# Kernel optimization log

Measured on AMD Instinct MI355X. Metric: run time of the kernel, lower is better.

Reference implementation:

```python
import math
import jax, jax.numpy as jnp
import numpy as np

B, T, E, H = 4, 2048, 1024, 16
D = E // H          # head_dim = 64
F = D // 2          # num_pairs = 32
FREQ_SIGMA = 1.0


def _build_spiral_frequencies(num_heads, num_pairs, freq_sigma):
    indices = np.arange(num_pairs, dtype=np.float32) + 0.5
    magnitudes = np.linspace(freq_sigma / max(num_pairs, 1), freq_sigma, num_pairs, dtype=np.float32)
    head_phases = np.linspace(0.0, 2.0 * math.pi, num_heads + 1, dtype=np.float32)[:-1][:, None]
    golden = (1.0 + math.sqrt(5.0)) / 2.0
    y = np.clip(1.0 - 2.0 * indices / float(num_pairs), -1.0, 1.0)
    radius = np.sqrt(np.clip(1.0 - y ** 2, 0.0, None))
    theta = (2.0 * math.pi * indices / golden)[None, :] + head_phases
    x = radius[None, :] * np.cos(theta)
    z = radius[None, :] * np.sin(theta)
    directions = np.stack([x, np.broadcast_to(y[None, :], (num_heads, num_pairs)), z], axis=-1)
    return (directions * magnitudes[None, :, None]).astype(np.float32)  # (H, F, 3)


def setup_inputs() -> dict:
    key = jax.random.key(0)
    ks = jax.random.split(key, 4)
    query = jax.random.normal(ks[0], (B, T, E), dtype=jnp.float32)
    positions = jax.random.normal(ks[1], (B, T, 3), dtype=jnp.float32)
    in_proj_weight = jax.random.normal(ks[2], (3 * E, E), dtype=jnp.float32) * (1.0 / math.sqrt(E))
    in_proj_bias = jnp.zeros((3 * E,), dtype=jnp.float32)
    out_proj_weight = jax.random.normal(ks[3], (E, E), dtype=jnp.float32) * (1.0 / math.sqrt(E))
    out_proj_bias = jnp.zeros((E,), dtype=jnp.float32)
    freqs = jnp.asarray(_build_spiral_frequencies(H, F, FREQ_SIGMA))
    return dict(query=query, positions=positions, in_proj_weight=in_proj_weight,
                in_proj_bias=in_proj_bias, out_proj_weight=out_proj_weight,
                out_proj_bias=out_proj_bias, freqs=freqs)


def _apply_rotary(x, positions, freqs):
    # x: (B, H, T, D), positions: (B, T, 3), freqs: (H, F, 3)
    angles = jnp.einsum('btd,hfd->bhtf', positions.astype(jnp.float32), freqs.astype(jnp.float32))
    cos = jnp.cos(angles).astype(x.dtype)
    sin = jnp.sin(angles).astype(x.dtype)
    xr = x.reshape(*x.shape[:-1], F, 2)
    x0, x1 = xr[..., 0], xr[..., 1]
    rotated = jnp.stack((x0 * cos - x1 * sin, x0 * sin + x1 * cos), axis=-1)
    return rotated.reshape(x.shape)  # rotary_dim == head_dim here


def reference(query, positions, in_proj_weight, in_proj_bias, out_proj_weight, out_proj_bias, freqs):
    b, t, e = query.shape
    h = freqs.shape[0]
    d = e // h
    # QKV projections (self-attention: all from query)
    q = query @ in_proj_weight[:e].T + in_proj_bias[:e]
    k = query @ in_proj_weight[e:2 * e].T + in_proj_bias[e:2 * e]
    v = query @ in_proj_weight[2 * e:].T + in_proj_bias[2 * e:]
    # split heads -> (B, H, T, D)
    q = q.reshape(b, t, h, d).transpose(0, 2, 1, 3)
    k = k.reshape(b, t, h, d).transpose(0, 2, 1, 3)
    v = v.reshape(b, t, h, d).transpose(0, 2, 1, 3)
    q = _apply_rotary(q, positions, freqs)
    k = _apply_rotary(k, positions, freqs)
    # SDPA
    scale = 1.0 / math.sqrt(d)
    scores = jnp.einsum('bhqd,bhkd->bhqk', q, k) * scale
    attn = jax.nn.softmax(scores, axis=-1)
    out = jnp.einsum('bhqk,bhkd->bhqd', attn, v)
    out = out.transpose(0, 2, 1, 3).reshape(b, t, e)
    return out @ out_proj_weight.T + out_proj_bias
```

## Files before the change

kernel.cpp:

```cpp
#include <hip/hip_runtime.h>
#include <math.h>

#define NB 4
#define NT 2048
#define NE 1024
#define NH 16
#define ND 64
#define NF 32

typedef _Float16 half8 __attribute__((ext_vector_type(8)));
typedef _Float16 half4 __attribute__((ext_vector_type(4)));
typedef _Float16 half2v __attribute__((ext_vector_type(2)));
typedef unsigned short ushort8v __attribute__((ext_vector_type(8)));
typedef unsigned int uint4v __attribute__((ext_vector_type(4)));
typedef float f32x4 __attribute__((ext_vector_type(4)));
typedef float f32x16 __attribute__((ext_vector_type(16)));
#define MFMA16(a, b, c) __builtin_amdgcn_mfma_f32_16x16x32_f16(a, b, c, 0, 0, 0)
#define MFMA32(a, b, c) __builtin_amdgcn_mfma_f32_32x32x16_f16(a, b, c, 0, 0, 0)

__device__ __forceinline__ float fast_exp2(float x) {
    float r;
    asm volatile("v_exp_f32 %0, %1" : "=v"(r) : "v"(x));
    return r;
}

__global__ __launch_bounds__(256)
void cvt_kernel(const float* __restrict__ X, const float* __restrict__ Wi,
                const float* __restrict__ Wo,
                _Float16* __restrict__ Xh, _Float16* __restrict__ Wih,
                _Float16* __restrict__ Woh)
{
    const size_t NX = (size_t)8388608, NWI = 3145728, NWO = 1048576;
    const size_t TOT = (NX + NWI + NWO) / 8;
    for (size_t gidx = (size_t)blockIdx.x*256 + threadIdx.x; gidx < TOT;
         gidx += (size_t)gridDim.x*256) {
        size_t i = gidx*8;
        const float* src; _Float16* dst; size_t off;
        if (i < NX)            { src = X;  dst = Xh;  off = i; }
        else if (i < NX + NWI) { src = Wi; dst = Wih; off = i - NX; }
        else                   { src = Wo; dst = Woh; off = i - NX - NWI; }
        float4 a = *(const float4*)(src + off);
        float4 b = *(const float4*)(src + off + 4);
        half8 h;
        h[0]=(_Float16)a.x; h[1]=(_Float16)a.y; h[2]=(_Float16)a.z; h[3]=(_Float16)a.w;
        h[4]=(_Float16)b.x; h[5]=(_Float16)b.y; h[6]=(_Float16)b.z; h[7]=(_Float16)b.w;
        *(half8*)(dst + off) = h;
    }
}

__global__ __launch_bounds__(256)
void qkv_mfma_kernel(const _Float16* __restrict__ Ah,
                     const _Float16* __restrict__ Bh,
                     const float* __restrict__ bias,
                     const float* __restrict__ pos,
                     const float* __restrict__ freqs,
                     _Float16* __restrict__ Qh,
                     _Float16* __restrict__ Kh,
                     _Float16* __restrict__ Vh)
{
    __shared__ _Float16 Ash[128*32];
    __shared__ _Float16 Bsh[128*32];

    const int tid = threadIdx.x;
    const int wid = tid >> 6, lane = tid & 63;
    const int ln = lane & 15, g = lane >> 4;
    const int wrow = wid >> 1, wcol = wid & 1;
    const int m0 = blockIdx.x * 128, n0 = blockIdx.y * 128;

    const int r0 = tid >> 2, s0 = tid & 3;
    const int k8 = s0 ^ ((r0 >> 1) & 3);
    const _Float16* gA0 = Ah + (size_t)(m0 + r0)      * NE + k8*8;
    const _Float16* gA1 = Ah + (size_t)(m0 + r0 + 64) * NE + k8*8;
    const _Float16* gB0 = Bh + (size_t)(n0 + r0)      * NE + k8*8;
    const _Float16* gB1 = Bh + (size_t)(n0 + r0 + 64) * NE + k8*8;

    const int xr = g ^ ((ln >> 1) & 3);

    f32x4 acc[4][4];
    #pragma unroll
    for (int i = 0; i < 4; ++i)
        #pragma unroll
        for (int j = 0; j < 4; ++j) acc[i][j] = (f32x4){0.f,0.f,0.f,0.f};

    half8 va0 = *(const half8*)gA0;
    half8 va1 = *(const half8*)gA1;
    half8 vb0 = *(const half8*)gB0;
    half8 vb1 = *(const half8*)gB1;

    for (int kt = 0; kt < NE; kt += 32) {
        if (kt) __syncthreads();
        *(half8*)&Ash[tid*8]       = va0;
        *(half8*)&Ash[(tid+256)*8] = va1;
        *(half8*)&Bsh[tid*8]       = vb0;
        *(half8*)&Bsh[(tid+256)*8] = vb1;
        __syncthreads();
        const int kn = kt + 32;
        if (kn < NE) {
            va0 = *(const half8*)(gA0 + kn);
            va1 = *(const half8*)(gA1 + kn);
            vb0 = *(const half8*)(gB0 + kn);
            vb1 = *(const half8*)(gB1 + kn);
        }
        half8 af[4], bf[4];
        #pragma unroll
        for (int mf = 0; mf < 4; ++mf)
            af[mf] = *(const half8*)&Ash[(wrow*64 + mf*16 + ln)*32 + xr*8];
        #pragma unroll
        for (int nf = 0; nf < 4; ++nf)
            bf[nf] = *(const half8*)&Bsh[(wcol*64 + nf*16 + ln)*32 + xr*8];
        __builtin_amdgcn_s_setprio(1);
        #pragma unroll
        for (int mf = 0; mf < 4; ++mf)
            #pragma unroll
            for (int nf = 0; nf < 4; ++nf)
                acc[mf][nf] = MFMA16(af[mf], bf[nf], acc[mf][nf]);
        __builtin_amdgcn_s_setprio(0);
    }

    const int sec = n0 >> 10;
    _Float16* dst = (sec == 0) ? Qh : (sec == 1) ? Kh : Vh;

    float cb[4], fx[4], fy[4], fz[4];
    int hh[4], dd[4];
    #pragma unroll
    for (int nf = 0; nf < 4; ++nf) {
        const int col = n0 + wcol*64 + nf*16 + ln;
        cb[nf] = bias[col];
        const int e = col & 1023;
        hh[nf] = e >> 6; dd[nf] = e & 63;
        if (sec != 2) {
            const float* fq = freqs + ((size_t)hh[nf]*NF + (dd[nf] >> 1))*3;
            fx[nf] = fq[0]; fy[nf] = fq[1]; fz[nf] = fq[2];
        }
    }
    const float sgn = (ln & 1) ? 1.0f : -1.0f;
    const float qs  = (sec == 0) ? 0.125f * 1.4426950408889634f : 1.0f;

    #pragma unroll
    for (int mf = 0; mf < 4; ++mf) {
        #pragma unroll
        for (int r = 0; r < 4; ++r) {
            const int m = m0 + wrow*64 + mf*16 + g*4 + r;
            const int b = m >> 11, t = m & 2047;
            if (sec == 2) {
                #pragma unroll
                for (int nf = 0; nf < 4; ++nf)
                    dst[((size_t)(b*NH + hh[nf])*NT + t)*ND + dd[nf]] =
                        (_Float16)(acc[mf][nf][r] + cb[nf]);
            } else {
                const float px = pos[(size_t)m*3 + 0];
                const float py = pos[(size_t)m*3 + 1];
                const float pz = pos[(size_t)m*3 + 2];
                #pragma unroll
                for (int nf = 0; nf < 4; ++nf) {
                    const float x  = acc[mf][nf][r] + cb[nf];
                    const float xo = __shfl_xor(x, 1);
                    const float ang = px*fx[nf] + py*fy[nf] + pz*fz[nf];
                    float sn, cs;
                    __sincosf(ang, &sn, &cs);
                    const float out = (x*cs + sgn*xo*sn) * qs;
                    dst[((size_t)(b*NH + hh[nf])*NT + t)*ND + dd[nf]] = (_Float16)out;
                }
            }
        }
    }
}

__global__ __launch_bounds__(256)
void attn_mfma_kernel(const _Float16* __restrict__ Qg, const _Float16* __restrict__ Kg,
                      const _Float16* __restrict__ Vg, _Float16* __restrict__ Og)
{
    __shared__ _Float16 Ks[64][68];
    __shared__ _Float16 VsT[64][68];

    const int tid  = threadIdx.x;
    const int wid  = tid >> 6;
    const int lane = tid & 63;
    const int m31  = lane & 31;
    const int hi   = lane >> 5;
    const int bh   = blockIdx.x;
    const int qt   = blockIdx.y;
    const int b = bh >> 4, h = bh & 15;
    const _Float16* Qp = Qg + (size_t)bh * NT * ND;
    const _Float16* Kp = Kg + (size_t)bh * NT * ND;
    const _Float16* Vp = Vg + (size_t)bh * NT * ND;

    const int qrow_g = qt*128 + wid*32 + m31;

    half8 qfr[4];
    #pragma unroll
    for (int c = 0; c < 4; ++c)
        qfr[c] = *(const half8*)(Qp + (size_t)qrow_g*ND + 16*c + 8*hi);

    f32x16 o[2];
    #pragma unroll
    for (int e = 0; e < 16; ++e) { o[0][e] = 0.f; o[1][e] = 0.f; }
    float m_i = -INFINITY, l_i = 0.0f;

    const int sr  = tid >> 2;
    const int sc0 = (tid & 3) * 16;
    const int dp  = tid & 31;
    const int wv  = tid >> 5;
    const _Float16* kbase = Kp + (size_t)sr*ND + sc0;
    const _Float16* vbase = Vp + (size_t)(wv*8)*ND + 2*dp;

    half8 kv0 = *(const half8*)(kbase);
    half8 kv1 = *(const half8*)(kbase + 8);
    unsigned int vr[8];
    #pragma unroll
    for (int j = 0; j < 8; ++j)
        vr[j] = *(const unsigned int*)(vbase + (size_t)j*ND);

    for (int kt = 0; kt < NT; kt += 64) {
        if (kt) __syncthreads();
        *(half8*)&Ks[sr][sc0]     = kv0;
        *(half8*)&Ks[sr][sc0 + 8] = kv1;
        {
            ushort8v lo, hiw;
            #pragma unroll
            for (int j = 0; j < 8; ++j) {
                lo[j]  = (unsigned short)(vr[j] & 0xffffu);
                hiw[j] = (unsigned short)(vr[j] >> 16);
            }
            *(ushort8v*)&VsT[2*dp][wv*8]     = lo;
            *(ushort8v*)&VsT[2*dp + 1][wv*8] = hiw;
        }
        __syncthreads();

        const int kn = kt + 64;
        if (kn < NT) {
            kv0 = *(const half8*)(kbase + (size_t)kn*ND);
            kv1 = *(const half8*)(kbase + (size_t)kn*ND + 8);
            #pragma unroll
            for (int j = 0; j < 8; ++j)
                vr[j] = *(const unsigned int*)(vbase + (size_t)(kn + j)*ND);
        }

        f32x16 st[2];
        #pragma unroll
        for (int e = 0; e < 16; ++e) { st[0][e] = 0.f; st[1][e] = 0.f; }

        __builtin_amdgcn_s_setprio(1);
        #pragma unroll
        for (int kb = 0; kb < 2; ++kb)
            #pragma unroll
            for (int c = 0; c < 4; ++c) {
                half8 kf = *(const half8*)&Ks[kb*32 + m31][16*c + 8*hi];
                st[kb] = MFMA32(kf, qfr[c], st[kb]);
            }
        __builtin_amdgcn_s_setprio(0);

        float pmax = st[0][0];
        #pragma unroll
        for (int e = 1; e < 16; ++e) pmax = fmaxf(pmax, st[0][e]);
        #pragma unroll
        for (int e = 0; e < 16; ++e) pmax = fmaxf(pmax, st[1][e]);
        pmax = fmaxf(pmax, __shfl_xor(pmax, 32));

        if (!__all(pmax - m_i <= 8.0f)) {
            const float mnew  = fmaxf(m_i, pmax);
            const float alpha = fast_exp2(m_i - mnew);
            m_i = mnew;
            l_i *= alpha;
            #pragma unroll
            for (int reg = 0; reg < 16; ++reg) {
                const int qr = (reg & 3) + 8*(reg >> 2) + 4*hi;
                const float a = __shfl(alpha, qr);
                o[0][reg] *= a;
                o[1][reg] *= a;
            }
        }

        float rs = 0.0f;
        unsigned int pku[2][8];
        #pragma unroll
        for (int kb = 0; kb < 2; ++kb)
            #pragma unroll
            for (int j = 0; j < 8; ++j) {
                const float p0 = fast_exp2(st[kb][2*j]     - m_i);
                const float p1 = fast_exp2(st[kb][2*j + 1] - m_i);
                rs += p0 + p1;
                pku[kb][j] = __builtin_bit_cast(unsigned int,
                               __builtin_amdgcn_cvt_pkrtz(p0, p1));
            }
        rs += __shfl_xor(rs, 32);
        l_i += rs;

        #pragma unroll
        for (int kc = 0; kc < 4; ++kc) {
            const int kb = kc >> 1;
            const unsigned int a0 = pku[kb][4*(kc & 1) + 0];
            const unsigned int a1 = pku[kb][4*(kc & 1) + 1];
            const unsigned int b0 = pku[kb][4*(kc & 1) + 2];
            const unsigned int b1 = pku[kb][4*(kc & 1) + 3];
            const unsigned int own0 = hi ? b0 : a0;
            const unsigned int own1 = hi ? b1 : a1;
            const unsigned int ex0  = hi ? a0 : b0;
            const unsigned int ex1  = hi ? a1 : b1;
            const unsigned int rc0 = __shfl_xor((int)ex0, 32);
            const unsigned int rc1 = __shfl_xor((int)ex1, 32);
            uint4v u;
            u.x = hi ? rc0 : own0;
            u.y = hi ? rc1 : own1;
            u.z = hi ? own0 : rc0;
            u.w = hi ? own1 : rc1;
            const half8 pa = __builtin_bit_cast(half8, u);
            const half8 vb0 = *(const half8*)&VsT[m31][16*kc + 8*hi];
            const half8 vb1 = *(const half8*)&VsT[32 + m31][16*kc + 8*hi];
            __builtin_amdgcn_s_setprio(1);
            o[0] = MFMA32(pa, vb0, o[0]);
            o[1] = MFMA32(pa, vb1, o[1]);
            __builtin_amdgcn_s_setprio(0);
        }
        __syncthreads();
    }

    #pragma unroll
    for (int reg = 0; reg < 16; ++reg) {
        const int qr = (reg & 3) + 8*(reg >> 2) + 4*hi;
        const float lq  = __shfl(l_i, qr);
        const float inv = 1.0f / lq;
        const int qg = qt*128 + wid*32 + qr;
        _Float16* dstp = Og + ((size_t)b*NT + qg)*NE + h*ND;
        dstp[m31]      = (_Float16)(o[0][reg] * inv);
        dstp[32 + m31] = (_Float16)(o[1][reg] * inv);
    }
}

__global__ __launch_bounds__(256)
void out_proj_mfma_kernel(const _Float16* __restrict__ Ah,
                          const _Float16* __restrict__ Bh,
                          const float* __restrict__ bias,
                          float* __restrict__ out)
{
    __shared__ _Float16 Ash[128*32];
    __shared__ _Float16 Bsh[128*32];

    const int tid = threadIdx.x;
    const int wid = tid >> 6, lane = tid & 63;
    const int ln = lane & 15, g = lane >> 4;
    const int wrow = wid >> 1, wcol = wid & 1;
    const int m0 = blockIdx.x * 128, n0 = blockIdx.y * 128;

    const int r0 = tid >> 2, s0 = tid & 3;
    const int k8 = s0 ^ ((r0 >> 1) & 3);
    const _Float16* gA0 = Ah + (size_t)(m0 + r0)      * NE + k8*8;
    const _Float16* gA1 = Ah + (size_t)(m0 + r0 + 64) * NE + k8*8;
    const _Float16* gB0 = Bh + (size_t)(n0 + r0)      * NE + k8*8;
    const _Float16* gB1 = Bh + (size_t)(n0 + r0 + 64) * NE + k8*8;
    const int xr = g ^ ((ln >> 1) & 3);

    f32x4 acc[4][4];
    #pragma unroll
    for (int i = 0; i < 4; ++i)
        #pragma unroll
        for (int j = 0; j < 4; ++j) acc[i][j] = (f32x4){0.f,0.f,0.f,0.f};

    half8 va0 = *(const half8*)gA0;
    half8 va1 = *(const half8*)gA1;
    half8 vb0 = *(const half8*)gB0;
    half8 vb1 = *(const half8*)gB1;

    for (int kt = 0; kt < NE; kt += 32) {
        if (kt) __syncthreads();
        *(half8*)&Ash[tid*8]       = va0;
        *(half8*)&Ash[(tid+256)*8] = va1;
        *(half8*)&Bsh[tid*8]       = vb0;
        *(half8*)&Bsh[(tid+256)*8] = vb1;
        __syncthreads();
        const int kn = kt + 32;
        if (kn < NE) {
            va0 = *(const half8*)(gA0 + kn);
            va1 = *(const half8*)(gA1 + kn);
            vb0 = *(const half8*)(gB0 + kn);
            vb1 = *(const half8*)(gB1 + kn);
        }
        half8 af[4], bf[4];
        #pragma unroll
        for (int mf = 0; mf < 4; ++mf)
            af[mf] = *(const half8*)&Ash[(wrow*64 + mf*16 + ln)*32 + xr*8];
        #pragma unroll
        for (int nf = 0; nf < 4; ++nf)
            bf[nf] = *(const half8*)&Bsh[(wcol*64 + nf*16 + ln)*32 + xr*8];
        __builtin_amdgcn_s_setprio(1);
        #pragma unroll
        for (int mf = 0; mf < 4; ++mf)
            #pragma unroll
            for (int nf = 0; nf < 4; ++nf)
                acc[mf][nf] = MFMA16(af[mf], bf[nf], acc[mf][nf]);
        __builtin_amdgcn_s_setprio(0);
    }

    float cb[4];
    #pragma unroll
    for (int nf = 0; nf < 4; ++nf) cb[nf] = bias[n0 + wcol*64 + nf*16 + ln];

    #pragma unroll
    for (int mf = 0; mf < 4; ++mf)
        #pragma unroll
        for (int r = 0; r < 4; ++r) {
            const int m = m0 + wrow*64 + mf*16 + g*4 + r;
            #pragma unroll
            for (int nf = 0; nf < 4; ++nf)
                out[(size_t)m*NE + n0 + wcol*64 + nf*16 + ln] = acc[mf][nf][r] + cb[nf];
        }
}

extern "C" void kernel_launch(void* const* d_in, const int* in_sizes, int n_in,
                              void* d_out, int out_size, void* d_ws, size_t ws_size,
                              hipStream_t stream)
{
    const float* X   = (const float*)d_in[0];
    const float* pos = (const float*)d_in[1];
    const float* Wi  = (const float*)d_in[2];
    const float* bi  = (const float*)d_in[3];
    const float* Wo  = (const float*)d_in[4];
    const float* bo  = (const float*)d_in[5];
    const float* fr  = (const float*)d_in[6];
    float* out = (float*)d_out;

    _Float16* Xh  = (_Float16*)d_ws;
    _Float16* Wih = Xh  + 8388608;
    _Float16* Woh = Wih + 3145728;
    _Float16* Qh  = Woh + 1048576;
    _Float16* Kh  = Qh  + 8388608;
    _Float16* Vh  = Kh  + 8388608;
    _Float16* Oh  = Vh  + 8388608;

    cvt_kernel          <<<3072, 256, 0, stream>>>(X, Wi, Wo, Xh, Wih, Woh);
    qkv_mfma_kernel     <<<dim3(64, 24), 256, 0, stream>>>(Xh, Wih, bi, pos, fr, Qh, Kh, Vh);
    attn_mfma_kernel    <<<dim3(64, 16), 256, 0, stream>>>(Qh, Kh, Vh, Oh);
    out_proj_mfma_kernel<<<dim3(64, 8),  256, 0, stream>>>(Oh, Woh, bo, out);
}
```

Measured before the change: 251.0 us.

## Double-buffer attention K/V shared tiles and streamline softmax inner loop

The attention kernel now keeps two shared-memory buffers for K and transposed V, so each iteration stores the next tile while computing on the current one, needing a single barrier per tile instead of two. The running max is folded into the MFMA accumulator initialisation, so the exp no longer needs a separate subtraction. The max reduction uses a three-input max tree, and the row sums use several independent accumulators. The half-wave probability exchange uses permlane32_swap and the V transpose uses byte permutes. These changes double the LDS footprint and change how the running max is tracked, starting from 8 instead of -inf.

```diff
diff --git a/kernel.cpp b/kernel.cpp
--- a/kernel.cpp
+++ b/kernel.cpp
@@ -10,8 +10,7 @@
 
 typedef _Float16 half8 __attribute__((ext_vector_type(8)));
 typedef _Float16 half4 __attribute__((ext_vector_type(4)));
-typedef _Float16 half2v __attribute__((ext_vector_type(2)));
-typedef unsigned short ushort8v __attribute__((ext_vector_type(8)));
+typedef unsigned int uint2v __attribute__((ext_vector_type(2)));
 typedef unsigned int uint4v __attribute__((ext_vector_type(4)));
 typedef float f32x4 __attribute__((ext_vector_type(4)));
 typedef float f32x16 __attribute__((ext_vector_type(16)));
@@ -22,6 +21,9 @@
     float r;
     asm volatile("v_exp_f32 %0, %1" : "=v"(r) : "v"(x));
     return r;
+}
+__device__ __forceinline__ float max3f(float a, float b, float c) {
+    return fmaxf(fmaxf(a, b), c);
 }
 
 __global__ __launch_bounds__(256)
@@ -170,8 +172,8 @@
 void attn_mfma_kernel(const _Float16* __restrict__ Qg, const _Float16* __restrict__ Kg,
                       const _Float16* __restrict__ Vg, _Float16* __restrict__ Og)
 {
-    __shared__ _Float16 Ks[64][68];
-    __shared__ _Float16 VsT[64][68];
+    __shared__ _Float16 Ks[2][64][68];
+    __shared__ _Float16 VsT[2][64][68];
 
     const int tid  = threadIdx.x;
     const int wid  = tid >> 6;
@@ -192,10 +194,10 @@
     for (int c = 0; c < 4; ++c)
         qfr[c] = *(const half8*)(Qp + (size_t)qrow_g*ND + 16*c + 8*hi);
 
-    f32x16 o[2];
-    #pragma unroll
-    for (int e = 0; e < 16; ++e) { o[0][e] = 0.f; o[1][e] = 0.f; }
-    float m_i = -INFINITY, l_i = 0.0f;
+    f32x16 o0, o1;
+    #pragma unroll
+    for (int e = 0; e < 16; ++e) { o0[e] = 0.f; o1[e] = 0.f; }
+    float m_i = 8.0f, l_i = 0.0f;
 
     const int sr  = tid >> 2;
     const int sc0 = (tid & 3) * 16;
@@ -204,115 +206,123 @@
     const _Float16* kbase = Kp + (size_t)sr*ND + sc0;
     const _Float16* vbase = Vp + (size_t)(wv*8)*ND + 2*dp;
 
-    half8 kv0 = *(const half8*)(kbase);
-    half8 kv1 = *(const half8*)(kbase + 8);
+    half8 kv0, kv1;
     unsigned int vr[8];
-    #pragma unroll
-    for (int j = 0; j < 8; ++j)
-        vr[j] = *(const unsigned int*)(vbase + (size_t)j*ND);
-
-    for (int kt = 0; kt < NT; kt += 64) {
-        if (kt) __syncthreads();
-        *(half8*)&Ks[sr][sc0]     = kv0;
-        *(half8*)&Ks[sr][sc0 + 8] = kv1;
-        {
-            ushort8v lo, hiw;
-            #pragma unroll
-            for (int j = 0; j < 8; ++j) {
-                lo[j]  = (unsigned short)(vr[j] & 0xffffu);
-                hiw[j] = (unsigned short)(vr[j] >> 16);
-            }
-            *(ushort8v*)&VsT[2*dp][wv*8]     = lo;
-            *(ushort8v*)&VsT[2*dp + 1][wv*8] = hiw;
-        }
+
+    #define LOADREGS(off)  do {                                              \
+        kv0 = *(const half8*)(kbase + (size_t)(off)*ND);                     \
+        kv1 = *(const half8*)(kbase + (size_t)(off)*ND + 8);                 \
+        _Pragma("unroll")                                                    \
+        for (int j = 0; j < 8; ++j)                                          \
+            vr[j] = *(const unsigned int*)(vbase + (size_t)((off) + j)*ND);  \
+    } while (0)
+
+    #define STOREBUF(bf)  do {                                               \
+        *(half8*)&Ks[bf][sr][sc0]     = kv0;                                 \
+        *(half8*)&Ks[bf][sr][sc0 + 8] = kv1;                                 \
+        uint4v lod, hid;                                                     \
+        _Pragma("unroll")                                                    \
+        for (int j2 = 0; j2 < 4; ++j2) {                                     \
+            lod[j2] = __builtin_amdgcn_perm(vr[2*j2+1], vr[2*j2], 0x05040100u); \
+            hid[j2] = __builtin_amdgcn_perm(vr[2*j2+1], vr[2*j2], 0x07060302u); \
+        }                                                                    \
+        *(uint4v*)&VsT[bf][2*dp][wv*8]     = lod;                            \
+        *(uint4v*)&VsT[bf][2*dp + 1][wv*8] = hid;                            \
+    } while (0)
+
+    LOADREGS(0);
+    STOREBUF(0);
+    LOADREGS(64);
+
+    for (int t = 0; t < 32; ++t) {
+        const int cur = t & 1;
         __syncthreads();
-
-        const int kn = kt + 64;
-        if (kn < NT) {
-            kv0 = *(const half8*)(kbase + (size_t)kn*ND);
-            kv1 = *(const half8*)(kbase + (size_t)kn*ND + 8);
-            #pragma unroll
-            for (int j = 0; j < 8; ++j)
-                vr[j] = *(const unsigned int*)(vbase + (size_t)(kn + j)*ND);
-        }
-
-        f32x16 st[2];
-        #pragma unroll
-        for (int e = 0; e < 16; ++e) { st[0][e] = 0.f; st[1][e] = 0.f; }
+        if (t < 31) STOREBUF(cur ^ 1);
+        if (t < 30) LOADREGS((t + 2) * 64);
+
+        f32x16 st0, st1;
+        const float mneg = -m_i;
+        #pragma unroll
+        for (int e = 0; e < 16; ++e) { st0[e] = mneg; st1[e] = mneg; }
 
         __builtin_amdgcn_s_setprio(1);
         #pragma unroll
-        for (int kb = 0; kb < 2; ++kb)
-            #pragma unroll
-            for (int c = 0; c < 4; ++c) {
-                half8 kf = *(const half8*)&Ks[kb*32 + m31][16*c + 8*hi];
-                st[kb] = MFMA32(kf, qfr[c], st[kb]);
-            }
+        for (int c = 0; c < 4; ++c) {
+            half8 kf0 = *(const half8*)&Ks[cur][m31][16*c + 8*hi];
+            half8 kf1 = *(const half8*)&Ks[cur][32 + m31][16*c + 8*hi];
+            st0 = MFMA32(kf0, qfr[c], st0);
+            st1 = MFMA32(kf1, qfr[c], st1);
+        }
         __builtin_amdgcn_s_setprio(0);
 
-        float pmax = st[0][0];
-        #pragma unroll
-        for (int e = 1; e < 16; ++e) pmax = fmaxf(pmax, st[0][e]);
-        #pragma unroll
-        for (int e = 0; e < 16; ++e) pmax = fmaxf(pmax, st[1][e]);
+        float t0 = max3f(st0[0],  st0[1],  st0[2]);
+        float t1 = max3f(st0[3],  st0[4],  st0[5]);
+        float t2 = max3f(st0[6],  st0[7],  st0[8]);
+        float t3 = max3f(st0[9],  st0[10], st0[11]);
+        float t4 = max3f(st0[12], st0[13], st0[14]);
+        float t5 = max3f(st0[15], st1[0],  st1[1]);
+        float t6 = max3f(st1[2],  st1[3],  st1[4]);
+        float t7 = max3f(st1[5],  st1[6],  st1[7]);
+        float t8 = max3f(st1[8],  st1[9],  st1[10]);
+        float t9 = max3f(st1[11], st1[12], st1[13]);
+        float ta = fmaxf(st1[14], st1[15]);
+        float u0 = max3f(t0, t1, t2);
+        float u1 = max3f(t3, t4, t5);
+        float u2 = max3f(t6, t7, t8);
+        float u3 = fmaxf(t9, ta);
+        float pmax = fmaxf(max3f(u0, u1, u2), u3);
         pmax = fmaxf(pmax, __shfl_xor(pmax, 32));
 
-        if (!__all(pmax - m_i <= 8.0f)) {
-            const float mnew  = fmaxf(m_i, pmax);
-            const float alpha = fast_exp2(m_i - mnew);
-            m_i = mnew;
+        if (!__all(pmax <= 8.0f)) {
+            const float delta = (pmax > 8.0f) ? pmax : 0.0f;
+            const float alpha = fast_exp2(-delta);
+            m_i += delta;
             l_i *= alpha;
             #pragma unroll
             for (int reg = 0; reg < 16; ++reg) {
                 const int qr = (reg & 3) + 8*(reg >> 2) + 4*hi;
                 const float a = __shfl(alpha, qr);
-                o[0][reg] *= a;
-                o[1][reg] *= a;
+                o0[reg] *= a; o1[reg] *= a;
             }
-        }
-
-        float rs = 0.0f;
-        unsigned int pku[2][8];
-        #pragma unroll
-        for (int kb = 0; kb < 2; ++kb)
             #pragma unroll
-            for (int j = 0; j < 8; ++j) {
-                const float p0 = fast_exp2(st[kb][2*j]     - m_i);
-                const float p1 = fast_exp2(st[kb][2*j + 1] - m_i);
-                rs += p0 + p1;
-                pku[kb][j] = __builtin_bit_cast(unsigned int,
-                               __builtin_amdgcn_cvt_pkrtz(p0, p1));
-            }
+            for (int e = 0; e < 16; ++e) { st0[e] -= delta; st1[e] -= delta; }
+        }
+
+        float r0 = 0.f, r1 = 0.f, r2 = 0.f, r3 = 0.f;
+        unsigned int pku0[8], pku1[8];
+        #pragma unroll
+        for (int j = 0; j < 8; ++j) {
+            const float pa0 = fast_exp2(st0[2*j]);
+            const float pa1 = fast_exp2(st0[2*j + 1]);
+            const float pb0 = fast_exp2(st1[2*j]);
+            const float pb1 = fast_exp2(st1[2*j + 1]);
+            if ((j & 1) == 0) { r0 += pa0 + pa1; r1 += pb0 + pb1; }
+            else              { r2 += pa0 + pa1; r3 += pb0 + pb1; }
+            pku0[j] = __builtin_bit_cast(unsigned int, __builtin_amdgcn_cvt_pkrtz(pa0, pa1));
+            pku1[j] = __builtin_bit_cast(unsigned int, __builtin_amdgcn_cvt_pkrtz(pb0, pb1));
+        }
+        float rs = (r0 + r1) + (r2 + r3);
         rs += __shfl_xor(rs, 32);
         l_i += rs;
 
         #pragma unroll
         for (int kc = 0; kc < 4; ++kc) {
-            const int kb = kc >> 1;
-            const unsigned int a0 = pku[kb][4*(kc & 1) + 0];
-            const unsigned int a1 = pku[kb][4*(kc & 1) + 1];
-            const unsigned int b0 = pku[kb][4*(kc & 1) + 2];
-            const unsigned int b1 = pku[kb][4*(kc & 1) + 3];
-            const unsigned int own0 = hi ? b0 : a0;
-            const unsigned int own1 = hi ? b1 : a1;
-            const unsigned int ex0  = hi ? a0 : b0;
-            const unsigned int ex1  = hi ? a1 : b1;
-            const unsigned int rc0 = __shfl_xor((int)ex0, 32);
-            const unsigned int rc1 = __shfl_xor((int)ex1, 32);
+            const unsigned int a0 = (kc < 2) ? pku0[4*(kc & 1) + 0] : pku1[4*(kc & 1) + 0];
+            const unsigned int a1 = (kc < 2) ? pku0[4*(kc & 1) + 1] : pku1[4*(kc & 1) + 1];
+            const unsigned int b0 = (kc < 2) ? pku0[4*(kc & 1) + 2] : pku1[4*(kc & 1) + 2];
+            const unsigned int b1 = (kc < 2) ? pku0[4*(kc & 1) + 3] : pku1[4*(kc & 1) + 3];
+            uint2v rpa = __builtin_amdgcn_permlane32_swap(a0, b0, false, false);
+            uint2v rpb = __builtin_amdgcn_permlane32_swap(a1, b1, false, false);
             uint4v u;
-            u.x = hi ? rc0 : own0;
-            u.y = hi ? rc1 : own1;
-            u.z = hi ? own0 : rc0;
-            u.w = hi ? own1 : rc1;
+            u[0] = rpa[0]; u[1] = rpb[0]; u[2] = rpa[1]; u[3] = rpb[1];
             const half8 pa = __builtin_bit_cast(half8, u);
-            const half8 vb0 = *(const half8*)&VsT[m31][16*kc + 8*hi];
-            const half8 vb1 = *(const half8*)&VsT[32 + m31][16*kc + 8*hi];
+            const half8 vb0 = *(const half8*)&VsT[cur][m31][16*kc + 8*hi];
+            const half8 vb1 = *(const half8*)&VsT[cur][32 + m31][16*kc + 8*hi];
             __builtin_amdgcn_s_setprio(1);
-            o[0] = MFMA32(pa, vb0, o[0]);
-            o[1] = MFMA32(pa, vb1, o[1]);
+            o0 = MFMA32(pa, vb0, o0);
+            o1 = MFMA32(pa, vb1, o1);
             __builtin_amdgcn_s_setprio(0);
         }
-        __syncthreads();
     }
 
     #pragma unroll
@@ -322,9 +332,11 @@
         const float inv = 1.0f / lq;
         const int qg = qt*128 + wid*32 + qr;
         _Float16* dstp = Og + ((size_t)b*NT + qg)*NE + h*ND;
-        dstp[m31]      = (_Float16)(o[0][reg] * inv);
-        dstp[32 + m31] = (_Float16)(o[1][reg] * inv);
-    }
+        dstp[m31]      = (_Float16)(o0[reg] * inv);
+        dstp[32 + m31] = (_Float16)(o1[reg] * inv);
+    }
+    #undef LOADREGS
+    #undef STOREBUF
 }
 
 __global__ __launch_bounds__(256)
```

Result: faster. 242.5 us (-3.4%).
